# Kernel tuning notes

Hardware: AMD Instinct MI355X
Metric: run time of the kernel (lower is better)

The kernel has to match this reference:

```python
import jax, jax.numpy as jnp
import numpy as np

D_MODEL = 128; D_STATE = 8; D_CONV = 4; D_INNER = 256; DT_RANK = 8
H1 = 32; INPUTS = 3; OUTPUTS = 5
B_SZ = 8; SEQ = 2048


def _mamba(u, in_proj_w, conv_w, conv_b, x_proj_w, dt_proj_w, dt_proj_b, A_log, Dp, out_proj_w):
    # u: [B, L, D_MODEL]
    B, L, _ = u.shape
    xz = u @ in_proj_w.T                      # [B, L, 2*D_INNER]
    xs, z = jnp.split(xz, 2, axis=-1)
    # depthwise causal conv1d over time
    xc = jnp.moveaxis(xs, 1, 2)               # [B, D_INNER, L]
    xc = jax.lax.conv_general_dilated(
        xc, conv_w, window_strides=(1,), padding=[(D_CONV - 1, 0)],
        feature_group_count=D_INNER, dimension_numbers=("NCH", "OIH", "NCH"))
    xc = xc + conv_b[None, :, None]
    xs = jax.nn.silu(jnp.moveaxis(xc, 1, 2))  # [B, L, D_INNER]
    x_dbl = xs @ x_proj_w.T                   # [B, L, DT_RANK + 2*D_STATE]
    dt = x_dbl[..., :DT_RANK]
    Bm = x_dbl[..., DT_RANK:DT_RANK + D_STATE]
    Cm = x_dbl[..., DT_RANK + D_STATE:]
    delta = jax.nn.softplus(dt @ dt_proj_w.T + dt_proj_b)   # [B, L, D_INNER]
    A = -jnp.exp(A_log)                                     # [D_INNER, D_STATE]
    dA = jnp.exp(jnp.einsum("bld,dn->bldn", delta, A))      # [B, L, D_INNER, D_STATE]
    dBu = jnp.einsum("bld,bln->bldn", delta * xs, Bm)       # delta * B * u

    def step(h, t):
        dA_t, dBu_t, C_t = t
        h = dA_t * h + dBu_t                  # [B, D_INNER, D_STATE]
        y = jnp.einsum("bdn,bn->bd", h, C_t)
        return h, y

    h0 = jnp.zeros((B, D_INNER, D_STATE), dA.dtype)
    _, ys = jax.lax.scan(step, h0, (jnp.moveaxis(dA, 1, 0), jnp.moveaxis(dBu, 1, 0), jnp.moveaxis(Cm, 1, 0)))
    y = jnp.moveaxis(ys, 0, 1) + Dp * xs      # [B, L, D_INNER]
    y = y * jax.nn.silu(z)
    return y @ out_proj_w.T                   # [B, L, D_MODEL]


def _forward(x, proj0_w, proj0_b, in_proj_w, conv_w, conv_b, x_proj_w, dt_proj_w, dt_proj_b,
             A_log, Dp, out_proj_w, mlin_w, mlin_b, proj1_w, proj1_b, lin1_w, lin1_b,
             proj2_w, proj2_b):
    out = x @ proj0_w.T + proj0_b                            # proj0
    out = jnp.tanh(out)                                      # Dropout(1e-4) -> eval identity; Tanh
    out = _mamba(out, in_proj_w, conv_w, conv_b, x_proj_w, dt_proj_w, dt_proj_b, A_log, Dp, out_proj_w)
    out = jax.nn.elu(out)
    mamba_out = out @ mlin_w.T + mlin_b                      # Linear(128,128)
    out = mamba_out @ proj1_w.T + proj1_b                    # proj1
    out = jax.nn.elu(out)
    out = out @ lin1_w.T + lin1_b                            # linear_seq
    combined = jnp.concatenate([x, mamba_out, out], axis=-1) # dstack -> [B, L, 3+128+32]
    o = combined @ proj2_w.T + proj2_b                       # [B, L, 5]
    PI = np.float32(np.pi)
    for _ in range(2):                                       # special_rounding_operation x2
        o = o + jnp.sin(o * PI) * 0.5
    o = (o + 1.0) * 0.5
    o = o.at[:, :, 2:].add(1.0)
    real = jnp.stack([
        x[:, :, 0] + o[:, :, 0],
        x[:, :, 1] + x[:, :, 2] * (o[:, :, 1] / o[:, :, 2]),
        x[:, :, 2] * (o[:, :, 3] / o[:, :, 4]),
    ], axis=-1)
    return real


def setup_inputs() -> dict:
    key = jax.random.key(0)
    ks = jax.random.split(key, 12)
    def w(k, shape, s=0.05):
        return (jax.random.normal(k, shape) * s).astype(jnp.float32)
    A_init = jnp.log(jnp.tile(jnp.arange(1, D_STATE + 1, dtype=jnp.float32), (D_INNER, 1)))
    return {
        "x": jax.random.normal(ks[0], (B_SZ, SEQ, INPUTS), dtype=jnp.float32),
        "proj0_w": w(ks[1], (D_MODEL, INPUTS)), "proj0_b": jnp.zeros((D_MODEL,), jnp.float32),
        "in_proj_w": w(ks[2], (2 * D_INNER, D_MODEL)),
        "conv_w": w(ks[3], (D_INNER, 1, D_CONV)), "conv_b": jnp.zeros((D_INNER,), jnp.float32),
        "x_proj_w": w(ks[4], (DT_RANK + 2 * D_STATE, D_INNER)),
        "dt_proj_w": w(ks[5], (D_INNER, DT_RANK)),
        "dt_proj_b": jnp.full((D_INNER,), -4.6, jnp.float32),
        "A_log": A_init, "Dp": jnp.ones((D_INNER,), jnp.float32),
        "out_proj_w": w(ks[6], (D_MODEL, D_INNER)),
        "mlin_w": w(ks[7], (D_MODEL, D_MODEL)), "mlin_b": jnp.zeros((D_MODEL,), jnp.float32),
        "proj1_w": w(ks[8], (H1, D_MODEL)), "proj1_b": jnp.zeros((H1,), jnp.float32),
        "lin1_w": w(ks[9], (H1, H1)), "lin1_b": jnp.zeros((H1,), jnp.float32),
        "proj2_w": w(ks[10], (OUTPUTS, INPUTS + D_MODEL + H1)),
        "proj2_b": jnp.zeros((OUTPUTS,), jnp.float32),
    }


def reference(x, proj0_w, proj0_b, in_proj_w, conv_w, conv_b, x_proj_w, dt_proj_w, dt_proj_b,
              A_log, Dp, out_proj_w, mlin_w, mlin_b, proj1_w, proj1_b, lin1_w, lin1_b,
              proj2_w, proj2_b):
    return _forward(x, proj0_w, proj0_b, in_proj_w, conv_w, conv_b, x_proj_w, dt_proj_w,
                    dt_proj_b, A_log, Dp, out_proj_w, mlin_w, mlin_b, proj1_w, proj1_b,
                    lin1_w, lin1_b, proj2_w, proj2_b)
```

## Files before the change

### kernel.cpp

```cpp
#include <hip/hip_runtime.h>
#include <hip/hip_bf16.h>
#include <math.h>

#define TOKENS 16384
#define SEQLEN 2048
#define NCHUNK 64
#define LCHUNK 32

typedef __attribute__((ext_vector_type(8))) short bf16x8;
typedef __attribute__((ext_vector_type(8))) unsigned short u16x8;
typedef __attribute__((ext_vector_type(4))) float f32x4;

__device__ inline unsigned short f2bf(float f) {
    unsigned u = __float_as_uint(f);
    return (unsigned short)((u + 0x7FFF + ((u >> 16) & 1)) >> 16);
}
__device__ inline float bf2f(unsigned short b) {
    return __uint_as_float((unsigned)b << 16);
}
__device__ inline f32x4 mfma16(bf16x8 a, bf16x8 b, f32x4 c) {
    return __builtin_amdgcn_mfma_f32_16x16x32_bf16(a, b, c, 0, 0, 0);
}
__device__ inline float fast_tanh(float x) {
    float ax = fabsf(x);
    float e = __expf(ax + ax);
    float r = 1.f - 2.f/(e + 1.f);
    return copysignf(r, x);
}

__global__ void k_prep2(const float* __restrict__ ipw, const float* __restrict__ opw,
                        const float* __restrict__ mlw,
                        const float* __restrict__ xpw, const float* __restrict__ dtw,
                        __hip_bfloat16* __restrict__ wi, __hip_bfloat16* __restrict__ wo,
                        __hip_bfloat16* __restrict__ wm, __hip_bfloat16* __restrict__ Wx) {
    int i = blockIdx.x * 256 + threadIdx.x;
    if (i < 65536) {
        int e = i;
        int chunk = e >> 9, ln = (e >> 3) & 63, j = e & 7;
        int g = chunk >> 4, kk = (chunk >> 2) & 3, w = chunk & 3;
        int r = ln & 15, q = ln >> 4;
        int row = g*64 + w*16 + r, col = kk*32 + q*8 + j;
        wi[i] = __float2bfloat16(ipw[row*128 + col]);
    } else if (i < 98304) {
        int e = i - 65536;
        int chunk = e >> 9, ln = (e >> 3) & 63, j = e & 7;
        int h = chunk >> 5, kk = (chunk >> 2) & 7, w = chunk & 3;
        int r = ln & 15, q = ln >> 4;
        int row = h*64 + w*16 + r, col = kk*32 + q*8 + j;
        wo[e] = __float2bfloat16(opw[row*256 + col]);
    } else if (i < 114688) {
        int e = i - 98304;
        int chunk = e >> 9, ln = (e >> 3) & 63, j = e & 7;
        int h = chunk >> 4, kk = (chunk >> 2) & 3, w = chunk & 3;
        int r = ln & 15, q = ln >> 4;
        int row = h*64 + w*16 + r, col = kk*32 + q*8 + j;
        wm[e] = __float2bfloat16(mlw[row*128 + col]);
    } else if (i < 196608) {
        int e = i - 114688;
        int chunk = e >> 9, ln = (e >> 3) & 63, j = e & 7;
        int g = chunk >> 5, kk = (chunk >> 2) & 7, w = chunk & 3;
        int r = ln & 15, q = ln >> 4;
        int n = g*64 + w*16 + r, k = kk*32 + q*8 + j;
        float v = 0.f;
        if (n < 256) {
            #pragma unroll
            for (int jj = 0; jj < 8; ++jj) v = fmaf(dtw[n*8+jj], xpw[jj*256+k], v);
        } else if (n < 272) {
            v = xpw[(n-248)*256 + k];
        }
        Wx[e] = __float2bfloat16(v);
    }
}

__global__ __launch_bounds__(256) void k_front(
    const float* __restrict__ x, const float* __restrict__ p0w,
    const float* __restrict__ p0b,
    const __hip_bfloat16* __restrict__ Wi,
    const __hip_bfloat16* __restrict__ Wx,
    const float* __restrict__ cw, const float* __restrict__ cb,
    const float* __restrict__ dpb, const float* __restrict__ A_log,
    __hip_bfloat16* __restrict__ zb,
    __hip_bfloat16* __restrict__ xsb,
    __hip_bfloat16* __restrict__ dlt,
    float* __restrict__ Bmo, float* __restrict__ Cmo,
    float* __restrict__ Ssum, unsigned short* __restrict__ Hend)
{
    __shared__ __align__(16) char smem[17408 + 17920];
    __shared__ float sx[48][3];
    __hip_bfloat16* U   = (__hip_bfloat16*)smem;
    __hip_bfloat16* AXS = (__hip_bfloat16*)smem;
    __hip_bfloat16* XCL = (__hip_bfloat16*)(smem + 17408);
    __hip_bfloat16* DL  = (__hip_bfloat16*)(smem + 17408);
    float* SB           = (float*)(smem + 17408 + 16896);

    int tid = threadIdx.x;
    int blk = blockIdx.x;
    int tok0 = blk * 32;
    bool seqstart = (tok0 & (SEQLEN-1)) == 0;

    if (tid < 144) {
        int row = tid/3, c = tid%3;
        int tok = tok0 - 16 + row;
        if (tok < 0) tok = 0;
        sx[row][c] = x[(size_t)tok*3 + c];
    }
    __syncthreads();
    {
        int col = tid & 127;
        int r0 = tid >> 7;
        float w0 = p0w[col*3+0], w1 = p0w[col*3+1], w2 = p0w[col*3+2];
        float b  = p0b[col];
        #pragma unroll
        for (int it = 0; it < 24; ++it) {
            int row = r0 + it*2;
            float v = b + sx[row][0]*w0 + sx[row][1]*w1 + sx[row][2]*w2;
            U[row*144 + col] = __float2bfloat16(fast_tanh(v));
        }
    }
    __syncthreads();

    int ln = tid & 63, w = tid >> 6;
    int r = ln & 15, q = ln >> 4;
    int ln8 = ln * 8;

    {
        f32x4 acch[4];
        #pragma unroll
        for (int g = 0; g < 4; ++g) acch[g] = (f32x4){0.f,0.f,0.f,0.f};
        const __hip_bfloat16* ah = &U[r*144 + q*8];
        #pragma unroll
        for (int kk = 0; kk < 4; ++kk) {
            bf16x8 a = *(const bf16x8*)(ah + kk*32);
            #pragma unroll
            for (int g = 0; g < 4; ++g) {
                bf16x8 bfv = *(const bf16x8*)(Wi + (((g*4 + kk)*4 + w) << 9) + ln8);
                acch[g] = mfma16(a, bfv, acch[g]);
            }
        }
        #pragma unroll
        for (int g = 0; g < 4; ++g) {
            int col = g*64 + w*16 + r;
            #pragma unroll
            for (int rr = 0; rr < 4; ++rr) {
                int row = q*4 + rr;
                if (row >= 13) {
                    int j = row - 13;
                    XCL[j*256 + col] = seqstart ? __float2bfloat16(0.f)
                                                : __float2bfloat16(acch[g][rr]);
                }
            }
        }
    }
    {
        f32x4 acc[2][8];
        #pragma unroll
        for (int mi = 0; mi < 2; ++mi)
            #pragma unroll
            for (int g = 0; g < 8; ++g) acc[mi][g] = (f32x4){0.f,0.f,0.f,0.f};
        const __hip_bfloat16* a0p = &U[(16+r)*144 + q*8];
        const __hip_bfloat16* a1p = &U[(32+r)*144 + q*8];
        #pragma unroll
        for (int kk = 0; kk < 4; ++kk) {
            bf16x8 a0 = *(const bf16x8*)(a0p + kk*32);
            bf16x8 a1 = *(const bf16x8*)(a1p + kk*32);
            #pragma unroll
            for (int g = 0; g < 8; ++g) {
                bf16x8 bfv = *(const bf16x8*)(Wi + (((g*4 + kk)*4 + w) << 9) + ln8);
                acc[0][g] = mfma16(a0, bfv, acc[0][g]);
                acc[1][g] = mfma16(a1, bfv, acc[1][g]);
            }
        }
        #pragma unroll
        for (int g = 0; g < 8; ++g) {
            int col = g*64 + w*16 + r;
            #pragma unroll
            for (int mi = 0; mi < 2; ++mi) {
                #pragma unroll
                for (int rr = 0; rr < 4; ++rr) {
                    int m = mi*16 + q*4 + rr;
                    float v = acc[mi][g][rr];
                    if (col < 256) XCL[(m+3)*256 + col] = __float2bfloat16(v);
                    else zb[(size_t)(tok0+m)*256 + col - 256] = __float2bfloat16(v);
                }
            }
        }
    }
    __syncthreads();

    {
        int d = tid;
        float cw0 = cw[d*4+0], cw1 = cw[d*4+1], cw2 = cw[d*4+2], cw3 = cw[d*4+3];
        float cbd = cb[d];
        #pragma unroll 4
        for (int row = 0; row < 32; ++row) {
            float acc = cbd;
            acc = fmaf(cw0, bf2f(*(const unsigned short*)&XCL[(row+0)*256 + d]), acc);
            acc = fmaf(cw1, bf2f(*(const unsigned short*)&XCL[(row+1)*256 + d]), acc);
            acc = fmaf(cw2, bf2f(*(const unsigned short*)&XCL[(row+2)*256 + d]), acc);
            acc = fmaf(cw3, bf2f(*(const unsigned short*)&XCL[(row+3)*256 + d]), acc);
            acc = acc / (1.f + __expf(-acc));
            __hip_bfloat16 hv = __float2bfloat16(acc);
            AXS[row*272 + d] = hv;
            xsb[(size_t)(tok0 + row)*256 + d] = hv;
        }
    }
    __syncthreads();

    {
        f32x4 acc[2][5];
        #pragma unroll
        for (int mi = 0; mi < 2; ++mi)
            #pragma unroll
            for (int g = 0; g < 5; ++g) acc[mi][g] = (f32x4){0.f,0.f,0.f,0.f};
        const __hip_bfloat16* arow0 = &AXS[r*272 + q*8];
        const __hip_bfloat16* arow1 = &AXS[(16+r)*272 + q*8];
        #pragma unroll
        for (int kk = 0; kk < 8; ++kk) {
            bf16x8 a0 = *(const bf16x8*)(arow0 + kk*32);
            bf16x8 a1 = *(const bf16x8*)(arow1 + kk*32);
            #pragma unroll
            for (int g = 0; g < 5; ++g) {
                bf16x8 bfv = *(const bf16x8*)(Wx + (((g*8 + kk)*4 + w) << 9) + ln8);
                acc[0][g] = mfma16(a0, bfv, acc[0][g]);
                acc[1][g] = mfma16(a1, bfv, acc[1][g]);
            }
        }
        #pragma unroll
        for (int g = 0; g < 5; ++g) {
            int col = g*64 + w*16 + r;
            if (col >= 272) continue;
            #pragma unroll
            for (int mi = 0; mi < 2; ++mi) {
                #pragma unroll
                for (int rr = 0; rr < 4; ++rr) {
                    int t = mi*16 + q*4 + rr;
                    int row = tok0 + t;
                    float v = acc[mi][g][rr];
                    if (col < 256) {
                        v += dpb[col];
                        v = (v > 20.f) ? v : log1pf(__expf(v));
                        __hip_bfloat16 hv = __float2bfloat16(v);
                        DL[t*264 + col] = hv;
                        dlt[(size_t)row*256 + col] = hv;
                    } else if (col < 264) {
                        SB[t*8 + col - 256] = v;
                        Bmo[(size_t)row*8 + col - 256] = v;
                    } else {
                        Cmo[(size_t)row*8 + col - 264] = v;
                    }
                }
            }
        }
    }
    __syncthreads();

    {
        int d = tid;
        float A[8];
        #pragma unroll
        for (int n = 0; n < 8; ++n) A[n] = -__expf(A_log[d*8+n]);
        float h[8] = {};
        float S = 0.f;
        for (int t = 0; t < LCHUNK; ++t) {
            float dt_c = bf2f(*(const unsigned short*)&DL[t*264 + d]);
            float xt_c = bf2f(*(const unsigned short*)&AXS[t*272 + d]);
            S += dt_c;
            float dx = dt_c * xt_c;
            #pragma unroll
            for (int n = 0; n < 8; ++n)
                h[n] = fmaf(__expf(A[n]*dt_c), h[n], dx * SB[t*8 + n]);
        }
        Ssum[(size_t)blk*256 + d] = S;
        u16x8 hp;
        #pragma unroll
        for (int n = 0; n < 8; ++n) hp[n] = f2bf(h[n]);
        *(u16x8*)&Hend[((size_t)blk*256 + d)*8] = hp;
    }
}

__global__ void k_scomb(const float* __restrict__ Ssum, const unsigned short* __restrict__ Hend,
                        const float* __restrict__ A_log, unsigned short* __restrict__ Hin) {
    int blk = blockIdx.x;
    int b = blk >> 3, dg = blk & 7;
    int d = dg*32 + (threadIdx.x >> 3);
    int n = threadIdx.x & 7;
    float A = -__expf(A_log[d*8+n]);
    float h = 0.f;
    size_t i0 = (size_t)(b*NCHUNK)*256 + d;
    float S  = Ssum[i0];
    float He = bf2f(Hend[i0*8 + n]);
    for (int c = 0; c < NCHUNK; ++c) {
        size_t idx = (size_t)(b*NCHUNK + c)*256 + d;
        float Sn = 0.f, Hn = 0.f;
        if (c < NCHUNK-1) {
            size_t ix2 = idx + 256;
            Sn = Ssum[ix2];
            Hn = bf2f(Hend[ix2*8 + n]);
        }
        Hin[idx*8 + n] = f2bf(h);
        h = fmaf(__expf(A*S), h, He);
        S = Sn; He = Hn;
    }
}

__global__ __launch_bounds__(256) void k_s2_opml(
    const __hip_bfloat16* __restrict__ delta,
    const __hip_bfloat16* __restrict__ xs,
    const float* __restrict__ Bm, const float* __restrict__ Cm,
    const __hip_bfloat16* __restrict__ zb,
    const float* __restrict__ A_log, const float* __restrict__ Dp,
    const unsigned short* __restrict__ Hin,
    const __hip_bfloat16* __restrict__ Wo,
    const __hip_bfloat16* __restrict__ Wm,
    const float* __restrict__ mlb,
    __hip_bfloat16* __restrict__ mo)
{
    __shared__ __hip_bfloat16 Al[32][272];
    __shared__ __hip_bfloat16 opl[32][136];
    __shared__ float sB[LCHUNK][8], sC[LCHUNK][8];
    int tid = threadIdx.x;
    int blk = blockIdx.x;
    int tok0 = blk * 32;
    {
        int t2 = tid >> 3, j = tid & 7;
        sB[t2][j] = Bm[(size_t)(tok0 + t2)*8 + j];
        sC[t2][j] = Cm[(size_t)(tok0 + t2)*8 + j];
    }
    int d = tid;
    float A[8], h[8];
    u16x8 hv = *(const u16x8*)&Hin[((size_t)blk*256 + d)*8];
    #pragma unroll
    for (int n = 0; n < 8; ++n) {
        A[n] = -__expf(A_log[d*8+n]);
        h[n] = bf2f(hv[n]);
    }
    float Dpd = Dp[d];
    __syncthreads();
    const __hip_bfloat16* dptr = delta + (size_t)tok0*256 + d;
    const __hip_bfloat16* xptr = xs    + (size_t)tok0*256 + d;
    const __hip_bfloat16* zptr = zb    + (size_t)tok0*256 + d;
    float dt_c = __bfloat162float(dptr[0]), xt_c = __bfloat162float(xptr[0]);
    for (int t = 0; t < LCHUNK; ++t) {
        float dt_n = 0.f, xt_n = 0.f;
        if (t < LCHUNK-1) {
            dt_n = __bfloat162float(dptr[(t+1)*256]);
            xt_n = __bfloat162float(xptr[(t+1)*256]);
        }
        float dx = dt_c * xt_c;
        float yv = 0.f;
        #pragma unroll
        for (int n = 0; n < 8; ++n) {
            h[n] = fmaf(__expf(A[n]*dt_c), h[n], dx * sB[t][n]);
            yv = fmaf(h[n], sC[t][n], yv);
        }
        yv = fmaf(Dpd, xt_c, yv);
        float z = __bfloat162float(zptr[t*256]);
        yv *= z / (1.f + __expf(-z));
        Al[t][d] = __float2bfloat16(yv);
        dt_c = dt_n; xt_c = xt_n;
    }
    __syncthreads();

    int ln = tid & 63, w = tid >> 6;
    int r = ln & 15, q = ln >> 4;
    int ln8 = ln * 8;
    int c0 = w*16 + r, c1 = c0 + 64;

    f32x4 a00 = (f32x4){0.f,0.f,0.f,0.f};
    f32x4 a01 = a00, a10 = a00, a11 = a00;
    const __hip_bfloat16* a0p = &Al[r][q*8];
    const __hip_bfloat16* a1p = &Al[16+r][q*8];
    #pragma unroll
    for (int kk = 0; kk < 8; ++kk) {
        bf16x8 af0 = *(const bf16x8*)(a0p + kk*32);
        bf16x8 af1 = *(const bf16x8*)(a1p + kk*32);
        bf16x8 bf0 = *(const bf16x8*)(Wo + (((0*8 + kk)*4 + w) << 9) + ln8);
        bf16x8 bf1 = *(const bf16x8*)(Wo + (((1*8 + kk)*4 + w) << 9) + ln8);
        a00 = mfma16(af0, bf0, a00);
        a10 = mfma16(af1, bf0, a10);
        a01 = mfma16(af0, bf1, a01);
        a11 = mfma16(af1, bf1, a11);
    }
    #pragma unroll
    for (int rr = 0; rr < 4; ++rr) {
        int row = q*4 + rr;
        float v;
        v = a00[rr]; v = v > 0.f ? v : (__expf(v)-1.f); opl[row][c0]    = __float2bfloat16(v);
        v = a01[rr]; v = v > 0.f ? v : (__expf(v)-1.f); opl[row][c1]    = __float2bfloat16(v);
        v = a10[rr]; v = v > 0.f ? v : (__expf(v)-1.f); opl[row+16][c0] = __float2bfloat16(v);
        v = a11[rr]; v = v > 0.f ? v : (__expf(v)-1.f); opl[row+16][c1] = __float2bfloat16(v);
    }
    __syncthreads();

    f32x4 m00 = (f32x4){0.f,0.f,0.f,0.f};
    f32x4 m01 = m00, m10 = m00, m11 = m00;
    const __hip_bfloat16* A0m = &opl[r][q*8];
    const __hip_bfloat16* A1m = &opl[16+r][q*8];
    #pragma unroll
    for (int kk = 0; kk < 4; ++kk) {
        bf16x8 af0 = *(const bf16x8*)(A0m + kk*32);
        bf16x8 af1 = *(const bf16x8*)(A1m + kk*32);
        bf16x8 bf0 = *(const bf16x8*)(Wm + (((0*4 + kk)*4 + w) << 9) + ln8);
        bf16x8 bf1 = *(const bf16x8*)(Wm + (((1*4 + kk)*4 + w) << 9) + ln8);
        m00 = mfma16(af0, bf0, m00);
        m10 = mfma16(af1, bf0, m10);
        m01 = mfma16(af0, bf1, m01);
        m11 = mfma16(af1, bf1, m11);
    }
    {
        float bl0 = mlb[c0], bl1 = mlb[c1];
        #pragma unroll
        for (int rr = 0; rr < 4; ++rr) {
            int row = q*4 + rr;
            mo[(size_t)(tok0+row)*128 + c0]    = __float2bfloat16(m00[rr] + bl0);
            mo[(size_t)(tok0+row)*128 + c1]    = __float2bfloat16(m01[rr] + bl1);
            mo[(size_t)(tok0+row+16)*128 + c0] = __float2bfloat16(m10[rr] + bl0);
            mo[(size_t)(tok0+row+16)*128 + c1] = __float2bfloat16(m11[rr] + bl1);
        }
    }
}

__global__ __launch_bounds__(256) void k_tail(const float* __restrict__ x,
                       const unsigned short* __restrict__ mo,
                       const float* __restrict__ p1w, const float* __restrict__ p1b,
                       const float* __restrict__ l1w, const float* __restrict__ l1b,
                       const float* __restrict__ p2w, const float* __restrict__ p2b,
                       float* __restrict__ out) {
    __shared__ float s_mo[16][132];
    __shared__ float s_p1w[32][132];
    __shared__ float s_l1w[32][36];
    __shared__ float s_p2w[5][164];
    __shared__ float s_h1[16][36];
    __shared__ float s_o32[16][36];
    __shared__ float s_o[16][6];
    int tid = threadIdx.x;
    int tok0 = blockIdx.x * 16;
    for (int i = tid; i < 32*32; i += 256) {
        int r = i >> 5, c = (i & 31) * 4;
        *(float4*)&s_p1w[r][c] = *(const float4*)&p1w[r*128 + c];
    }
    for (int i = tid; i < 32*8; i += 256) {
        int r = i >> 3, c = (i & 7) * 4;
        *(float4*)&s_l1w[r][c] = *(const float4*)&l1w[r*32 + c];
    }
    for (int i = tid; i < 5*163; i += 256)
        s_p2w[i / 163][i % 163] = p2w[i];
    {
        int i = tid;
        int r = i >> 4, c = (i & 15) * 8;
        u16x8 v = *(const u16x8*)&mo[(size_t)(tok0 + r)*128 + c];
        #pragma unroll
        for (int e = 0; e < 8; ++e) s_mo[r][c+e] = bf2f(v[e]);
    }
    __syncthreads();
    {
        int j = tid & 31, tb = tid >> 5;
        float bj = p1b[j];
        #pragma unroll
        for (int p = 0; p < 2; ++p) {
            int tk = tb + p*8;
            float v = bj;
            #pragma unroll 8
            for (int k = 0; k < 128; k += 4) {
                float4 m4 = *(const float4*)&s_mo[tk][k];
                float4 w4 = *(const float4*)&s_p1w[j][k];
                v = fmaf(m4.x, w4.x, v); v = fmaf(m4.y, w4.y, v);
                v = fmaf(m4.z, w4.z, v); v = fmaf(m4.w, w4.w, v);
            }
            v = v > 0.f ? v : (__expf(v) - 1.f);
            s_h1[tk][j] = v;
        }
    }
    __syncthreads();
    {
        int j = tid & 31, tb = tid >> 5;
        float bj = l1b[j];
        #pragma unroll
        for (int p = 0; p < 2; ++p) {
            int tk = tb + p*8;
            float v = bj;
            #pragma unroll
            for (int k = 0; k < 32; k += 4) {
                float4 m4 = *(const float4*)&s_h1[tk][k];
                float4 w4 = *(const float4*)&s_l1w[j][k];
                v = fmaf(m4.x, w4.x, v); v = fmaf(m4.y, w4.y, v);
                v = fmaf(m4.z, w4.z, v); v = fmaf(m4.w, w4.w, v);
            }
            s_o32[tk][j] = v;
        }
    }
    __syncthreads();
    if (tid < 160) {
        int tk = tid / 10, rem = tid % 10;
        int j = rem >> 1, half = rem & 1;
        const float* wr = s_p2w[j];
        float v = 0.f;
        if (half == 0) {
            int tok = tok0 + tk;
            v = fmaf(x[tok*3+0], wr[0], v);
            v = fmaf(x[tok*3+1], wr[1], v);
            v = fmaf(x[tok*3+2], wr[2], v);
            #pragma unroll 8
            for (int k = 0; k < 64; ++k) v = fmaf(s_mo[tk][k], wr[3+k], v);
        } else {
            #pragma unroll 8
            for (int k = 64; k < 128; ++k) v = fmaf(s_mo[tk][k], wr[3+k], v);
            #pragma unroll 8
            for (int k = 0; k < 32; ++k)  v = fmaf(s_o32[tk][k], wr[131+k], v);
        }
        v += __shfl_xor(v, 1);
        if (half == 0) {
            v += p2b[j];
            const float PI = 3.14159265358979323846f;
            v = v + __sinf(v*PI)*0.5f;
            v = v + __sinf(v*PI)*0.5f;
            v = (v + 1.f)*0.5f;
            if (j >= 2) v += 1.f;
            s_o[tk][j] = v;
        }
    }
    __syncthreads();
    if (tid < 48) {
        int tk = tid / 3, ln = tid % 3;
        int tok = tok0 + tk;
        float x0 = x[tok*3+0], x1 = x[tok*3+1], x2 = x[tok*3+2];
        float r;
        if (ln == 0)      r = x0 + s_o[tk][0];
        else if (ln == 1) r = x1 + x2*(s_o[tk][1]/s_o[tk][2]);
        else              r = x2*(s_o[tk][3]/s_o[tk][4]);
        out[(size_t)tok*3 + ln] = r;
    }
}

extern "C" void kernel_launch(void* const* d_in, const int* in_sizes, int n_in,
                              void* d_out, int out_size, void* d_ws, size_t ws_size,
                              hipStream_t stream) {
    const float* x        = (const float*)d_in[0];
    const float* proj0_w  = (const float*)d_in[1];
    const float* proj0_b  = (const float*)d_in[2];
    const float* in_proj_w= (const float*)d_in[3];
    const float* conv_w   = (const float*)d_in[4];
    const float* conv_b   = (const float*)d_in[5];
    const float* x_proj_w = (const float*)d_in[6];
    const float* dt_proj_w= (const float*)d_in[7];
    const float* dt_proj_b= (const float*)d_in[8];
    const float* A_log    = (const float*)d_in[9];
    const float* Dp       = (const float*)d_in[10];
    const float* out_proj_w=(const float*)d_in[11];
    const float* mlin_w   = (const float*)d_in[12];
    const float* mlin_b   = (const float*)d_in[13];
    const float* proj1_w  = (const float*)d_in[14];
    const float* proj1_b  = (const float*)d_in[15];
    const float* lin1_w   = (const float*)d_in[16];
    const float* lin1_b   = (const float*)d_in[17];
    const float* proj2_w  = (const float*)d_in[18];
    const float* proj2_b  = (const float*)d_in[19];
    float* out = (float*)d_out;

    char* wsb = (char*)d_ws;
    const size_t MB = 1048576;
    __hip_bfloat16* z_bf   = (__hip_bfloat16*)(wsb + 12*MB);
    __hip_bfloat16* xs_bf  = (__hip_bfloat16*)(wsb + 20*MB);
    __hip_bfloat16* dlt_bf = (__hip_bfloat16*)(wsb + 28*MB);
    float* Bm   = (float*)(wsb + 36*MB);
    float* Cm   = (float*)(wsb + 36*MB + 524288);
    float* Ssum = (float*)(wsb + 37*MB);
    unsigned short* Hend = (unsigned short*)(wsb + 37*MB + 524288);
    unsigned short* Hin  = (unsigned short*)(wsb + 39*MB + 524288);
    __hip_bfloat16* w_in_bf  = (__hip_bfloat16*)(wsb + 50*MB);
    __hip_bfloat16* w_out_bf = (__hip_bfloat16*)(wsb + 50*MB + 131072);
    __hip_bfloat16* w_ml_bf  = (__hip_bfloat16*)(wsb + 50*MB + 196608);
    __hip_bfloat16* Wx_bf    = (__hip_bfloat16*)(wsb + 50*MB + 229376);
    unsigned short* mo = (unsigned short*)(wsb + 51*MB);

    k_prep2<<<768, 256, 0, stream>>>(in_proj_w, out_proj_w, mlin_w, x_proj_w,
                                     dt_proj_w, w_in_bf, w_out_bf, w_ml_bf, Wx_bf);
    k_front<<<TOKENS/32, 256, 0, stream>>>(x, proj0_w, proj0_b, w_in_bf, Wx_bf,
                                           conv_w, conv_b, dt_proj_b, A_log,
                                           z_bf, xs_bf, dlt_bf, Bm, Cm, Ssum, Hend);
    k_scomb<<<64, 256, 0, stream>>>(Ssum, Hend, A_log, Hin);
    k_s2_opml<<<TOKENS/32, 256, 0, stream>>>(dlt_bf, xs_bf, Bm, Cm, z_bf, A_log, Dp,
                                             Hin, w_out_bf, w_ml_bf, mlin_b,
                                             (__hip_bfloat16*)mo);
    k_tail<<<TOKENS/16, 256, 0, stream>>>(x, mo, proj1_w, proj1_b, lin1_w, lin1_b, proj2_w, proj2_b, out);
}
```

Before: 93.82 us.

## Transpose conv and scan staging buffers to channel-major with vectorized access

Shared-memory staging buffers for the conv input, delta and xs move to channel-major (transposed) layouts, so each thread can load its whole time series with a few vector reads into registers. The xs workspace in global memory is also stored per block in channel-major order, which lets the second scan kernel load it with 16-byte vector reads. The scan loops are fully unrolled over the chunk. Shared memory grows from about 35KB to about 56KB per block, which can lower occupancy, and register pressure rises from the unrolled register arrays.

Result: slower. 112.9 us (+20.3%).

```diff
diff --git a/kernel.cpp b/kernel.cpp
--- a/kernel.cpp
+++ b/kernel.cpp
@@ -9,6 +9,7 @@
 
 typedef __attribute__((ext_vector_type(8))) short bf16x8;
 typedef __attribute__((ext_vector_type(8))) unsigned short u16x8;
+typedef __attribute__((ext_vector_type(4))) unsigned short u16x4;
 typedef __attribute__((ext_vector_type(4))) float f32x4;
 
 __device__ inline unsigned short f2bf(float f) {
@@ -80,23 +81,29 @@
     const float* __restrict__ cw, const float* __restrict__ cb,
     const float* __restrict__ dpb, const float* __restrict__ A_log,
     __hip_bfloat16* __restrict__ zb,
-    __hip_bfloat16* __restrict__ xsb,
+    __hip_bfloat16* __restrict__ xsg,
     __hip_bfloat16* __restrict__ dlt,
     float* __restrict__ Bmo, float* __restrict__ Cmo,
     float* __restrict__ Ssum, unsigned short* __restrict__ Hend)
 {
-    __shared__ __align__(16) char smem[17408 + 17920];
+    __shared__ __align__(16) char smem[56320];
     __shared__ float sx[48][3];
-    __hip_bfloat16* U   = (__hip_bfloat16*)smem;
-    __hip_bfloat16* AXS = (__hip_bfloat16*)smem;
-    __hip_bfloat16* XCL = (__hip_bfloat16*)(smem + 17408);
-    __hip_bfloat16* DL  = (__hip_bfloat16*)(smem + 17408);
-    float* SB           = (float*)(smem + 17408 + 16896);
+    __shared__ float SB[LCHUNK][8];
+    __hip_bfloat16* U    = (__hip_bfloat16*)smem;
+    __hip_bfloat16* AXS  = (__hip_bfloat16*)smem;
+    unsigned short* XCT  = (unsigned short*)(smem + 17408);
+    unsigned short* DLT  = (unsigned short*)(smem + 17408);
+    unsigned short* XST  = (unsigned short*)(smem + 37888);
 
     int tid = threadIdx.x;
     int blk = blockIdx.x;
     int tok0 = blk * 32;
     bool seqstart = (tok0 & (SEQLEN-1)) == 0;
+
+    __hip_bfloat16* zbb  = zb  + (size_t)tok0*256;
+    __hip_bfloat16* dltb = dlt + (size_t)tok0*256;
+    float* Bmb = Bmo + (size_t)tok0*8;
+    float* Cmb = Cmo + (size_t)tok0*8;
 
     if (tid < 144) {
         int row = tid/3, c = tid%3;
@@ -144,9 +151,8 @@
             for (int rr = 0; rr < 4; ++rr) {
                 int row = q*4 + rr;
                 if (row >= 13) {
-                    int j = row - 13;
-                    XCL[j*256 + col] = seqstart ? __float2bfloat16(0.f)
-                                                : __float2bfloat16(acch[g][rr]);
+                    XCT[col*40 + (row - 12)] = seqstart ? (unsigned short)0
+                                                        : f2bf(acch[g][rr]);
                 }
             }
         }
@@ -172,16 +178,22 @@
         }
         #pragma unroll
         for (int g = 0; g < 8; ++g) {
-            int col = g*64 + w*16 + r;
-            #pragma unroll
-            for (int mi = 0; mi < 2; ++mi) {
+            if (g < 4) {
+                int col = g*64 + w*16 + r;
                 #pragma unroll
-                for (int rr = 0; rr < 4; ++rr) {
-                    int m = mi*16 + q*4 + rr;
-                    float v = acc[mi][g][rr];
-                    if (col < 256) XCL[(m+3)*256 + col] = __float2bfloat16(v);
-                    else zb[(size_t)(tok0+m)*256 + col - 256] = __float2bfloat16(v);
+                for (int mi = 0; mi < 2; ++mi) {
+                    u16x4 pk;
+                    #pragma unroll
+                    for (int rr = 0; rr < 4; ++rr) pk[rr] = f2bf(acc[mi][g][rr]);
+                    *(u16x4*)&XCT[col*40 + mi*16 + q*4 + 4] = pk;
                 }
+            } else {
+                int zc = (g-4)*64 + w*16 + r;
+                #pragma unroll
+                for (int mi = 0; mi < 2; ++mi)
+                    #pragma unroll
+                    for (int rr = 0; rr < 4; ++rr)
+                        zbb[(mi*16 + q*4 + rr)*256 + zc] = __float2bfloat16(acc[mi][g][rr]);
             }
         }
     }
@@ -189,19 +201,42 @@
 
     {
         int d = tid;
-        float cw0 = cw[d*4+0], cw1 = cw[d*4+1], cw2 = cw[d*4+2], cw3 = cw[d*4+3];
+        float4 cwv = *(const float4*)&cw[d*4];
         float cbd = cb[d];
-        #pragma unroll 4
+        u16x4 xrv[9];
+        #pragma unroll
+        for (int k = 0; k < 9; ++k) xrv[k] = *(const u16x4*)&XCT[d*40 + k*4];
+        float xf[36];
+        #pragma unroll
+        for (int j = 1; j < 36; ++j) xf[j] = bf2f(xrv[j>>2][j&3]);
+        unsigned short hs[32];
+        __hip_bfloat16* AXSp = AXS;
+        #pragma unroll
         for (int row = 0; row < 32; ++row) {
             float acc = cbd;
-            acc = fmaf(cw0, bf2f(*(const unsigned short*)&XCL[(row+0)*256 + d]), acc);
-            acc = fmaf(cw1, bf2f(*(const unsigned short*)&XCL[(row+1)*256 + d]), acc);
-            acc = fmaf(cw2, bf2f(*(const unsigned short*)&XCL[(row+2)*256 + d]), acc);
-            acc = fmaf(cw3, bf2f(*(const unsigned short*)&XCL[(row+3)*256 + d]), acc);
+            acc = fmaf(cwv.x, xf[row+1], acc);
+            acc = fmaf(cwv.y, xf[row+2], acc);
+            acc = fmaf(cwv.z, xf[row+3], acc);
+            acc = fmaf(cwv.w, xf[row+4], acc);
             acc = acc / (1.f + __expf(-acc));
-            __hip_bfloat16 hv = __float2bfloat16(acc);
-            AXS[row*272 + d] = hv;
-            xsb[(size_t)(tok0 + row)*256 + d] = hv;
+            unsigned short hv = f2bf(acc);
+            hs[row] = hv;
+            AXSp[row*272 + d] = *(__hip_bfloat16*)&hv;
+        }
+        #pragma unroll
+        for (int k = 0; k < 8; ++k) {
+            u16x4 st;
+            #pragma unroll
+            for (int j = 0; j < 4; ++j) st[j] = hs[k*4+j];
+            *(u16x4*)&XST[d*36 + k*4] = st;
+        }
+        unsigned short* xg = (unsigned short*)xsg + (size_t)blk*8192 + d*32;
+        #pragma unroll
+        for (int k = 0; k < 4; ++k) {
+            u16x8 st;
+            #pragma unroll
+            for (int j = 0; j < 8; ++j) st[j] = hs[k*8+j];
+            *(u16x8*)&xg[k*8] = st;
         }
     }
     __syncthreads();
@@ -234,19 +269,18 @@
                 #pragma unroll
                 for (int rr = 0; rr < 4; ++rr) {
                     int t = mi*16 + q*4 + rr;
-                    int row = tok0 + t;
                     float v = acc[mi][g][rr];
                     if (col < 256) {
                         v += dpb[col];
                         v = (v > 20.f) ? v : log1pf(__expf(v));
-                        __hip_bfloat16 hv = __float2bfloat16(v);
-                        DL[t*264 + col] = hv;
-                        dlt[(size_t)row*256 + col] = hv;
+                        unsigned short hv = f2bf(v);
+                        DLT[col*36 + t] = hv;
+                        dltb[t*256 + col] = *(__hip_bfloat16*)&hv;
                     } else if (col < 264) {
-                        SB[t*8 + col - 256] = v;
-                        Bmo[(size_t)row*8 + col - 256] = v;
+                        SB[t][col - 256] = v;
+                        Bmb[t*8 + col - 256] = v;
                     } else {
-                        Cmo[(size_t)row*8 + col - 264] = v;
+                        Cmb[t*8 + col - 264] = v;
                     }
                 }
             }
@@ -256,19 +290,28 @@
 
     {
         int d = tid;
+        float4 al0 = *(const float4*)&A_log[d*8];
+        float4 al1 = *(const float4*)&A_log[d*8+4];
         float A[8];
-        #pragma unroll
-        for (int n = 0; n < 8; ++n) A[n] = -__expf(A_log[d*8+n]);
+        A[0]=-__expf(al0.x); A[1]=-__expf(al0.y); A[2]=-__expf(al0.z); A[3]=-__expf(al0.w);
+        A[4]=-__expf(al1.x); A[5]=-__expf(al1.y); A[6]=-__expf(al1.z); A[7]=-__expf(al1.w);
+        u16x4 drv[8], xrv2[8];
+        #pragma unroll
+        for (int k = 0; k < 8; ++k) {
+            drv[k]  = *(const u16x4*)&DLT[d*36 + k*4];
+            xrv2[k] = *(const u16x4*)&XST[d*36 + k*4];
+        }
         float h[8] = {};
         float S = 0.f;
+        #pragma unroll
         for (int t = 0; t < LCHUNK; ++t) {
-            float dt_c = bf2f(*(const unsigned short*)&DL[t*264 + d]);
-            float xt_c = bf2f(*(const unsigned short*)&AXS[t*272 + d]);
+            float dt_c = bf2f(drv[t>>2][t&3]);
+            float xt_c = bf2f(xrv2[t>>2][t&3]);
             S += dt_c;
             float dx = dt_c * xt_c;
             #pragma unroll
             for (int n = 0; n < 8; ++n)
-                h[n] = fmaf(__expf(A[n]*dt_c), h[n], dx * SB[t*8 + n]);
+                h[n] = fmaf(__expf(A[n]*dt_c), h[n], dx * SB[t][n]);
         }
         Ssum[(size_t)blk*256 + d] = S;
         u16x8 hp;
@@ -305,7 +348,7 @@
 
 __global__ __launch_bounds__(256) void k_s2_opml(
     const __hip_bfloat16* __restrict__ delta,
-    const __hip_bfloat16* __restrict__ xs,
+    const __hip_bfloat16* __restrict__ xst,
     const float* __restrict__ Bm, const float* __restrict__ Cm,
     const __hip_bfloat16* __restrict__ zb,
     const float* __restrict__ A_log, const float* __restrict__ Dp,
@@ -327,25 +370,28 @@
         sC[t2][j] = Cm[(size_t)(tok0 + t2)*8 + j];
     }
     int d = tid;
+    float4 al0 = *(const float4*)&A_log[d*8];
+    float4 al1 = *(const float4*)&A_log[d*8+4];
     float A[8], h[8];
+    A[0]=-__expf(al0.x); A[1]=-__expf(al0.y); A[2]=-__expf(al0.z); A[3]=-__expf(al0.w);
+    A[4]=-__expf(al1.x); A[5]=-__expf(al1.y); A[6]=-__expf(al1.z); A[7]=-__expf(al1.w);
     u16x8 hv = *(const u16x8*)&Hin[((size_t)blk*256 + d)*8];
     #pragma unroll
-    for (int n = 0; n < 8; ++n) {
-        A[n] = -__expf(A_log[d*8+n]);
-        h[n] = bf2f(hv[n]);
-    }
+    for (int n = 0; n < 8; ++n) h[n] = bf2f(hv[n]);
     float Dpd = Dp[d];
+    u16x8 xv[4];
+    {
+        const unsigned short* xg = (const unsigned short*)xst + (size_t)blk*8192 + d*32;
+        #pragma unroll
+        for (int k = 0; k < 4; ++k) xv[k] = *(const u16x8*)&xg[k*8];
+    }
     __syncthreads();
     const __hip_bfloat16* dptr = delta + (size_t)tok0*256 + d;
-    const __hip_bfloat16* xptr = xs    + (size_t)tok0*256 + d;
     const __hip_bfloat16* zptr = zb    + (size_t)tok0*256 + d;
-    float dt_c = __bfloat162float(dptr[0]), xt_c = __bfloat162float(xptr[0]);
+    #pragma unroll
     for (int t = 0; t < LCHUNK; ++t) {
-        float dt_n = 0.f, xt_n = 0.f;
-        if (t < LCHUNK-1) {
-            dt_n = __bfloat162float(dptr[(t+1)*256]);
-            xt_n = __bfloat162float(xptr[(t+1)*256]);
-        }
+        float dt_c = __bfloat162float(dptr[t*256]);
+        float xt_c = bf2f(xv[t>>3][t&7]);
         float dx = dt_c * xt_c;
         float yv = 0.f;
         #pragma unroll
@@ -357,7 +403,6 @@
         float z = __bfloat162float(zptr[t*256]);
         yv *= z / (1.f + __expf(-z));
         Al[t][d] = __float2bfloat16(yv);
-        dt_c = dt_n; xt_c = xt_n;
     }
     __syncthreads();
 
@@ -409,13 +454,14 @@
     }
     {
         float bl0 = mlb[c0], bl1 = mlb[c1];
+        __hip_bfloat16* mob = mo + (size_t)tok0*128;
         #pragma unroll
         for (int rr = 0; rr < 4; ++rr) {
             int row = q*4 + rr;
-            mo[(size_t)(tok0+row)*128 + c0]    = __float2bfloat16(m00[rr] + bl0);
-            mo[(size_t)(tok0+row)*128 + c1]    = __float2bfloat16(m01[rr] + bl1);
-            mo[(size_t)(tok0+row+16)*128 + c0] = __float2bfloat16(m10[rr] + bl0);
-            mo[(size_t)(tok0+row+16)*128 + c1] = __float2bfloat16(m11[rr] + bl1);
+            mob[row*128 + c0]      = __float2bfloat16(m00[rr] + bl0);
+            mob[row*128 + c1]      = __float2bfloat16(m01[rr] + bl1);
+            mob[(row+16)*128 + c0] = __float2bfloat16(m10[rr] + bl0);
+            mob[(row+16)*128 + c1] = __float2bfloat16(m11[rr] + bl1);
         }
     }
 }
@@ -560,7 +606,7 @@
     char* wsb = (char*)d_ws;
     const size_t MB = 1048576;
     __hip_bfloat16* z_bf   = (__hip_bfloat16*)(wsb + 12*MB);
-    __hip_bfloat16* xs_bf  = (__hip_bfloat16*)(wsb + 20*MB);
+    __hip_bfloat16* xs_t   = (__hip_bfloat16*)(wsb + 20*MB);
     __hip_bfloat16* dlt_bf = (__hip_bfloat16*)(wsb + 28*MB);
     float* Bm   = (float*)(wsb + 36*MB);
     float* Cm   = (float*)(wsb + 36*MB + 524288);
@@ -577,9 +623,9 @@
                                      dt_proj_w, w_in_bf, w_out_bf, w_ml_bf, Wx_bf);
     k_front<<<TOKENS/32, 256, 0, stream>>>(x, proj0_w, proj0_b, w_in_bf, Wx_bf,
                                            conv_w, conv_b, dt_proj_b, A_log,
-                                           z_bf, xs_bf, dlt_bf, Bm, Cm, Ssum, Hend);
+                                           z_bf, xs_t, dlt_bf, Bm, Cm, Ssum, Hend);
     k_scomb<<<64, 256, 0, stream>>>(Ssum, Hend, A_log, Hin);
-    k_s2_opml<<<TOKENS/32, 256, 0, stream>>>(dlt_bf, xs_bf, Bm, Cm, z_bf, A_log, Dp,
+    k_s2_opml<<<TOKENS/32, 256, 0, stream>>>(dlt_bf, xs_t, Bm, Cm, z_bf, A_log, Dp,
                                              Hin, w_out_bf, w_ml_bf, mlin_b,
                                              (__hip_bfloat16*)mo);
     k_tail<<<TOKENS/16, 256, 0, stream>>>(x, mo, proj1_w, proj1_b, lin1_w, lin1_b, proj2_w, proj2_b, out);
```
